# Kernel tuning notes

Hardware: AMD Instinct MI355X
Metric: run time of the kernel (lower is better)

## Reference

```python
import jax, jax.numpy as jnp
import numpy as np

N_NODES = 50000
N_REL = 1000
N_EDGES = 1600000
F_OUT = 64
N_HEAD = 2
NEG_SLOPE = 0.2


def setup_inputs() -> dict:
    key = jax.random.key(0)
    k_h, k_r, k_a0, k_a1, k_a2, k_w, k_att = jax.random.split(key, 7)
    h = jax.random.normal(k_h, (N_NODES, F_OUT), dtype=jnp.float32)
    inputr = jax.random.normal(k_r, (N_REL, F_OUT), dtype=jnp.float32)
    # A[0]=dst node, A[1]=relation id, A[2]=src node
    a0 = jax.random.randint(k_a0, (N_EDGES,), 0, N_NODES, dtype=jnp.int32)
    a1 = jax.random.randint(k_a1, (N_EDGES,), 0, N_REL, dtype=jnp.int32)
    a2 = jax.random.randint(k_a2, (N_EDGES,), 0, N_NODES, dtype=jnp.int32)
    A = jnp.stack([a0, a1, a2], axis=0)
    # params: w ~ diag per-head scale, a_src_dst ~ N(0, 1/sqrt(2*f_out))
    w = jax.random.normal(k_w, (N_HEAD - 1, 1, F_OUT), dtype=jnp.float32)
    stdv = 1.0 / np.sqrt(2 * F_OUT)
    a_src_dst = (jax.random.normal(k_att, (N_HEAD, 2, F_OUT, 1), dtype=jnp.float32) * stdv)
    return {"h": h, "inputr": inputr, "A": A, "w": w, "a_src_dst": a_src_dst}


def reference(h, inputr, A, w, a_src_dst):
    N = h.shape[0]
    dst, rel_idx, src_idx = A[0], A[1], A[2]
    outs = []
    for i in range(N_HEAD):
        if i >= 1:
            h = h * w[i - 1]  # cumulative diag rescale across heads
        src = h[src_idx]          # [E, f] gather
        rel = inputr[rel_idx]     # [E, f] gather
        score = src @ a_src_dst[i, 0] + rel @ a_src_dst[i, 1]  # [E, 1]
        edge_e = jnp.exp(-jax.nn.leaky_relu(score[:, 0], NEG_SLOPE))  # [E]
        rowsum = jax.ops.segment_sum(edge_e, dst, num_segments=N)[:, None]  # [N,1]
        msg = (src - rel) * edge_e[:, None]  # [E, f]
        h_prime = jax.ops.segment_sum(msg, dst, num_segments=N) / rowsum
        outs.append(h_prime)
    return jnp.stack(outs, axis=0)  # [n_head, N, f]
```

## Files before the change

### kernel.cpp

```cpp
#include <hip/hip_runtime.h>
#include <hip/hip_fp16.h>

#define NNODES 50000
#define NREL   1000
#define NEDGES 1600000
#define FOUT   64
#define NEG_SLOPE 0.2f

#define SPAN   16
#define NBUCK  3125
#define CAP    704
#define PTHR   1024
#define EPT    16
#define CHUNK  (PTHR * EPT)
#define DBLK   98
#define PREB   797


#define ALIGN1K(x) (((x) + 1023) & ~((size_t)1023))
static const size_t OFF_HS    = 0;
static const size_t OFF_RR    = ALIGN1K(OFF_HS    + sizeof(float2) * NNODES);
static const size_t OFF_CNT   = ALIGN1K(OFF_RR    + sizeof(float2) * NREL);
static const size_t OFF_H16   = ALIGN1K(OFF_CNT   + sizeof(int) * NBUCK);
static const size_t OFF_R16   = ALIGN1K(OFF_H16   + sizeof(unsigned short) * NNODES * FOUT);
static const size_t OFF_STAGE = ALIGN1K(OFF_R16   + sizeof(unsigned short) * NREL * FOUT);

__global__ __launch_bounds__(PTHR) void prep_kernel(
    const float* __restrict__ h, const float* __restrict__ inputr,
    const float* __restrict__ w, const float* __restrict__ a_att,
    const int* __restrict__ A, int* __restrict__ ccnt, int* __restrict__ stage,
    float2* __restrict__ hs2, float2* __restrict__ rr2,
    unsigned short* __restrict__ h16, unsigned short* __restrict__ r16)
{
    const int t = threadIdx.x;
    if (blockIdx.x < DBLK) {
        __shared__ int lcnt[NBUCK];
        __shared__ int gbase[NBUCK];
        for (int i = t; i < NBUCK; i += PTHR) lcnt[i] = 0;
        __syncthreads();

        const int base = blockIdx.x * CHUNK;
        int rec[EPT];
        short bkt[EPT];
        int off[EPT];

        #pragma unroll
        for (int k = 0; k < EPT; k++) {
            const int e = base + k * PTHR + t;
            if (e < NEDGES) {
                const int dn = __builtin_nontemporal_load(A + e);
                const int rn = __builtin_nontemporal_load(A + NEDGES + e);
                const int sn = __builtin_nontemporal_load(A + 2 * NEDGES + e);
                const int b  = dn >> 4;
                rec[k] = ((dn & 15) << 26) | (sn << 10) | rn;
                bkt[k] = (short)b;
                off[k] = atomicAdd(&lcnt[b], 1);
            } else {
                off[k] = -1;
            }
        }
        __syncthreads();

        for (int i = t; i < NBUCK; i += PTHR) {
            const int c = lcnt[i];
            if (c > 0) gbase[i] = i * CAP + atomicAdd(&ccnt[i], c);
        }
        __syncthreads();

        #pragma unroll
        for (int k = 0; k < EPT; k++) {
            if (off[k] >= 0) {
                const int b   = bkt[k];
                const int pos = gbase[b] + off[k];
                if (pos < (b + 1) * CAP)
                    stage[pos] = rec[k];
            }
        }
        return;
    }

    const int lane = t & 15;
    const int f0   = lane << 2;
    const int g    = (blockIdx.x - DBLK) * 64 + (t >> 4);
    if (g >= NNODES + NREL) return;

    const float4 a00 = *(const float4*)(a_att +   0 + f0);
    const float4 a01 = *(const float4*)(a_att +  64 + f0);
    const float4 a10 = *(const float4*)(a_att + 128 + f0);
    const float4 a11 = *(const float4*)(a_att + 192 + f0);
    const float4 wv  = *(const float4*)(w + f0);

    float p0, p1;
    float4 v;
    if (g < NNODES) {
        v = *(const float4*)(h + (size_t)g * FOUT + f0);
        p0 = v.x * a00.x + v.y * a00.y + v.z * a00.z + v.w * a00.w;
        p1 = v.x * wv.x * a10.x + v.y * wv.y * a10.y
           + v.z * wv.z * a10.z + v.w * wv.w * a10.w;
    } else {
        v = *(const float4*)(inputr + (size_t)(g - NNODES) * FOUT + f0);
        p0 = v.x * a01.x + v.y * a01.y + v.z * a01.z + v.w * a01.w;
        p1 = v.x * a11.x + v.y * a11.y + v.z * a11.z + v.w * a11.w;
    }

    {
        ushort4 pk;
        pk.x = __half_as_ushort(__float2half(v.x));
        pk.y = __half_as_ushort(__float2half(v.y));
        pk.z = __half_as_ushort(__float2half(v.z));
        pk.w = __half_as_ushort(__float2half(v.w));
        if (g < NNODES) *(ushort4*)(h16 + (size_t)g * FOUT + f0) = pk;
        else            *(ushort4*)(r16 + (size_t)(g - NNODES) * FOUT + f0) = pk;
    }

    #pragma unroll
    for (int off = 8; off >= 1; off >>= 1) {
        p0 += __shfl_xor(p0, off, 16);
        p1 += __shfl_xor(p1, off, 16);
    }
    if (lane == 0) {
        if (g < NNODES) hs2[g] = make_float2(p0, p1);
        else            rr2[g - NNODES] = make_float2(p0, p1);
    }
}

__global__ __launch_bounds__(256) void sortagg_kernel(
    const unsigned short* __restrict__ h16, const unsigned short* __restrict__ r16,
    const float* __restrict__ w,
    const int* __restrict__ stage, const int* __restrict__ ccnt,
    const float2* __restrict__ hs2, const float2* __restrict__ rr2,
    float* __restrict__ out)
{
    __shared__ int    lsort[CAP];
    __shared__ float2 ew[CAP];
    __shared__ int hist[SPAN];
    __shared__ int offs[SPAN];
    __shared__ int sstart[SPAN + 1];

    const int b = blockIdx.x;
    const int t = threadIdx.x;
    int cnt = ccnt[b];
    if (cnt > CAP) cnt = CAP;
    const int base = b * CAP;

    if (t < SPAN) hist[t] = 0;
    __syncthreads();

    for (int i = t; i < cnt; i += 256)
        atomicAdd(&hist[((unsigned)stage[base + i]) >> 26], 1);
    __syncthreads();

    if (t < SPAN) {
        const int c = hist[t];
        int v = c;
        #pragma unroll
        for (int d = 1; d < SPAN; d <<= 1) {
            const int u = __shfl_up(v, d);
            if (t >= d) v += u;
        }
        sstart[t] = v - c;
        offs[t]   = v - c;
        if (t == SPAN - 1) sstart[SPAN] = v;
    }
    __syncthreads();

    for (int i = t; i < cnt; i += 256) {
        const int r = stage[base + i];
        const int pos = atomicAdd(&offs[((unsigned)r) >> 26], 1);
        lsort[pos] = r;
        const int sn = (r >> 10) & 0xFFFF;
        const int rn = r & 1023;
        const float2 hv = hs2[sn];
        const float2 rv = rr2[rn];
        const float sc0 = hv.x + rv.x;
        const float sc1 = hv.y + rv.y;
        ew[pos] = make_float2(__expf(-fmaxf(sc0, NEG_SLOPE * sc0)),
                              __expf(-fmaxf(sc1, NEG_SLOPE * sc1)));
    }
    __syncthreads();

    const int wv  = t >> 6;
    const int oct = (t & 63) >> 3;
    const int f8  = (t & 7) << 3;
    const float4 wl0 = *(const float4*)(w + f8);
    const float4 wl1 = *(const float4*)(w + f8 + 4);

    for (int nl = wv; nl < SPAN; nl += 4) {
        const int node = b * SPAN + nl;
        const int s0 = sstart[nl];
        const int s1 = sstart[nl + 1];

        float4 a0l = make_float4(0.f, 0.f, 0.f, 0.f);
        float4 a0h = make_float4(0.f, 0.f, 0.f, 0.f);
        float4 a1l = make_float4(0.f, 0.f, 0.f, 0.f);
        float4 a1h = make_float4(0.f, 0.f, 0.f, 0.f);
        float sum0 = 0.f, sum1 = 0.f;

        for (int i = s0 + oct; i < s1; i += 8) {
            const int p     = lsort[i];
            const float2 ee = ew[i];
            const int sn = (p >> 10) & 0xFFFF;
            const int rn = p & 1023;

            const uint4 su = *(const uint4*)(h16 + ((size_t)sn << 6) + f8);
            const uint4 ru = *(const uint4*)(r16 + ((size_t)rn << 6) + f8);
            const float2 s01 = __half22float2(__builtin_bit_cast(__half2, su.x));
            const float2 s23 = __half22float2(__builtin_bit_cast(__half2, su.y));
            const float2 s45 = __half22float2(__builtin_bit_cast(__half2, su.z));
            const float2 s67 = __half22float2(__builtin_bit_cast(__half2, su.w));
            const float2 r01 = __half22float2(__builtin_bit_cast(__half2, ru.x));
            const float2 r23 = __half22float2(__builtin_bit_cast(__half2, ru.y));
            const float2 r45 = __half22float2(__builtin_bit_cast(__half2, ru.z));
            const float2 r67 = __half22float2(__builtin_bit_cast(__half2, ru.w));

            a0l.x += (s01.x - r01.x) * ee.x;
            a0l.y += (s01.y - r01.y) * ee.x;
            a0l.z += (s23.x - r23.x) * ee.x;
            a0l.w += (s23.y - r23.y) * ee.x;
            a0h.x += (s45.x - r45.x) * ee.x;
            a0h.y += (s45.y - r45.y) * ee.x;
            a0h.z += (s67.x - r67.x) * ee.x;
            a0h.w += (s67.y - r67.y) * ee.x;
            a1l.x += fmaf(s01.x, wl0.x, -r01.x) * ee.y;
            a1l.y += fmaf(s01.y, wl0.y, -r01.y) * ee.y;
            a1l.z += fmaf(s23.x, wl0.z, -r23.x) * ee.y;
            a1l.w += fmaf(s23.y, wl0.w, -r23.y) * ee.y;
            a1h.x += fmaf(s45.x, wl1.x, -r45.x) * ee.y;
            a1h.y += fmaf(s45.y, wl1.y, -r45.y) * ee.y;
            a1h.z += fmaf(s67.x, wl1.z, -r67.x) * ee.y;
            a1h.w += fmaf(s67.y, wl1.w, -r67.y) * ee.y;
            sum0 += ee.x;
            sum1 += ee.y;
        }

        #pragma unroll
        for (int off = 8; off <= 32; off <<= 1) {
            a0l.x += __shfl_xor(a0l.x, off);
            a0l.y += __shfl_xor(a0l.y, off);
            a0l.z += __shfl_xor(a0l.z, off);
            a0l.w += __shfl_xor(a0l.w, off);
            a0h.x += __shfl_xor(a0h.x, off);
            a0h.y += __shfl_xor(a0h.y, off);
            a0h.z += __shfl_xor(a0h.z, off);
            a0h.w += __shfl_xor(a0h.w, off);
            a1l.x += __shfl_xor(a1l.x, off);
            a1l.y += __shfl_xor(a1l.y, off);
            a1l.z += __shfl_xor(a1l.z, off);
            a1l.w += __shfl_xor(a1l.w, off);
            a1h.x += __shfl_xor(a1h.x, off);
            a1h.y += __shfl_xor(a1h.y, off);
            a1h.z += __shfl_xor(a1h.z, off);
            a1h.w += __shfl_xor(a1h.w, off);
            sum0   += __shfl_xor(sum0, off);
            sum1   += __shfl_xor(sum1, off);
        }

        if (oct == 0) {
            const float inv = 1.0f / sum0;
            float* o = out + (size_t)node * FOUT + f8;
            *(float4*)(o)     = make_float4(a0l.x * inv, a0l.y * inv, a0l.z * inv, a0l.w * inv);
            *(float4*)(o + 4) = make_float4(a0h.x * inv, a0h.y * inv, a0h.z * inv, a0h.w * inv);
        } else if (oct == 1) {
            const float inv = 1.0f / sum1;
            float* o = out + ((size_t)NNODES + node) * FOUT + f8;
            *(float4*)(o)     = make_float4(a1l.x * inv, a1l.y * inv, a1l.z * inv, a1l.w * inv);
            *(float4*)(o + 4) = make_float4(a1h.x * inv, a1h.y * inv, a1h.z * inv, a1h.w * inv);
        }
    }
}

extern "C" void kernel_launch(void* const* d_in, const int* in_sizes, int n_in,
                              void* d_out, int out_size, void* d_ws, size_t ws_size,
                              hipStream_t stream) {
    const float* h      = (const float*)d_in[0];
    const float* inputr = (const float*)d_in[1];
    const int*   A      = (const int*)d_in[2];
    const float* w      = (const float*)d_in[3];
    const float* a_att  = (const float*)d_in[4];

    char* ws = (char*)d_ws;
    float2*         hs2   = (float2*)(ws + OFF_HS);
    float2*         rr2   = (float2*)(ws + OFF_RR);
    int*            ccnt  = (int*)(ws + OFF_CNT);
    unsigned short* h16   = (unsigned short*)(ws + OFF_H16);
    unsigned short* r16   = (unsigned short*)(ws + OFF_R16);
    int*            stage = (int*)(ws + OFF_STAGE);
    float*          out   = (float*)d_out;

    hipMemsetAsync(ccnt, 0, sizeof(int) * NBUCK, stream);

    prep_kernel<<<dim3(DBLK + PREB), dim3(PTHR), 0, stream>>>(
        h, inputr, w, a_att, A, ccnt, stage, hs2, rr2, h16, r16);
    sortagg_kernel<<<dim3(NBUCK), dim3(256), 0, stream>>>(
        h16, r16, w, stage, ccnt, hs2, rr2, out);
}
```

Measured before the change: 88.45 us.

## Halve sortagg block size and unroll edge loop by two for more loads in flight

The aggregation kernel now runs 128-thread blocks (2 wavefronts per 16-node bucket, each handling 8 nodes) with a min-blocks-per-CU launch hint. The inner edge loop is unrolled by two so each thread issues four 16-byte gathers before consuming them, raising memory-level parallelism. The smaller block halves the threads doing the shared-memory bucket sort and makes each wave process twice as many nodes, trading thread parallelism for more blocks resident per CU. The extra in-flight loads increase register use, which the launch-bounds hint constrains.

```diff
diff --git a/kernel.cpp b/kernel.cpp
--- a/kernel.cpp
+++ b/kernel.cpp
@@ -124,7 +124,7 @@
     }
 }
 
-__global__ __launch_bounds__(256) void sortagg_kernel(
+__global__ __launch_bounds__(128, 7) void sortagg_kernel(
     const unsigned short* __restrict__ h16, const unsigned short* __restrict__ r16,
     const float* __restrict__ w,
     const int* __restrict__ stage, const int* __restrict__ ccnt,
@@ -146,7 +146,7 @@
     if (t < SPAN) hist[t] = 0;
     __syncthreads();
 
-    for (int i = t; i < cnt; i += 256)
+    for (int i = t; i < cnt; i += 128)
         atomicAdd(&hist[((unsigned)stage[base + i]) >> 26], 1);
     __syncthreads();
 
@@ -164,7 +164,7 @@
     }
     __syncthreads();
 
-    for (int i = t; i < cnt; i += 256) {
+    for (int i = t; i < cnt; i += 128) {
         const int r = stage[base + i];
         const int pos = atomicAdd(&offs[((unsigned)r) >> 26], 1);
         lsort[pos] = r;
@@ -185,7 +185,7 @@
     const float4 wl0 = *(const float4*)(w + f8);
     const float4 wl1 = *(const float4*)(w + f8 + 4);
 
-    for (int nl = wv; nl < SPAN; nl += 4) {
+    for (int nl = wv; nl < SPAN; nl += 2) {
         const int node = b * SPAN + nl;
         const int s0 = sstart[nl];
         const int s1 = sstart[nl + 1];
@@ -196,12 +196,82 @@
         float4 a1h = make_float4(0.f, 0.f, 0.f, 0.f);
         float sum0 = 0.f, sum1 = 0.f;
 
-        for (int i = s0 + oct; i < s1; i += 8) {
+        int i = s0 + oct;
+        for (; i + 8 < s1; i += 16) {
+            const int pA     = lsort[i];
+            const float2 eA  = ew[i];
+            const int pB     = lsort[i + 8];
+            const float2 eB  = ew[i + 8];
+            const int snA = (pA >> 10) & 0xFFFF, rnA = pA & 1023;
+            const int snB = (pB >> 10) & 0xFFFF, rnB = pB & 1023;
+
+            const uint4 suA = *(const uint4*)(h16 + ((size_t)snA << 6) + f8);
+            const uint4 ruA = *(const uint4*)(r16 + ((size_t)rnA << 6) + f8);
+            const uint4 suB = *(const uint4*)(h16 + ((size_t)snB << 6) + f8);
+            const uint4 ruB = *(const uint4*)(r16 + ((size_t)rnB << 6) + f8);
+
+            {
+                const float2 s01 = __half22float2(__builtin_bit_cast(__half2, suA.x));
+                const float2 s23 = __half22float2(__builtin_bit_cast(__half2, suA.y));
+                const float2 s45 = __half22float2(__builtin_bit_cast(__half2, suA.z));
+                const float2 s67 = __half22float2(__builtin_bit_cast(__half2, suA.w));
+                const float2 r01 = __half22float2(__builtin_bit_cast(__half2, ruA.x));
+                const float2 r23 = __half22float2(__builtin_bit_cast(__half2, ruA.y));
+                const float2 r45 = __half22float2(__builtin_bit_cast(__half2, ruA.z));
+                const float2 r67 = __half22float2(__builtin_bit_cast(__half2, ruA.w));
+                a0l.x += (s01.x - r01.x) * eA.x;
+                a0l.y += (s01.y - r01.y) * eA.x;
+                a0l.z += (s23.x - r23.x) * eA.x;
+                a0l.w += (s23.y - r23.y) * eA.x;
+                a0h.x += (s45.x - r45.x) * eA.x;
+                a0h.y += (s45.y - r45.y) * eA.x;
+                a0h.z += (s67.x - r67.x) * eA.x;
+                a0h.w += (s67.y - r67.y) * eA.x;
+                a1l.x += fmaf(s01.x, wl0.x, -r01.x) * eA.y;
+                a1l.y += fmaf(s01.y, wl0.y, -r01.y) * eA.y;
+                a1l.z += fmaf(s23.x, wl0.z, -r23.x) * eA.y;
+                a1l.w += fmaf(s23.y, wl0.w, -r23.y) * eA.y;
+                a1h.x += fmaf(s45.x, wl1.x, -r45.x) * eA.y;
+                a1h.y += fmaf(s45.y, wl1.y, -r45.y) * eA.y;
+                a1h.z += fmaf(s67.x, wl1.z, -r67.x) * eA.y;
+                a1h.w += fmaf(s67.y, wl1.w, -r67.y) * eA.y;
+                sum0 += eA.x;
+                sum1 += eA.y;
+            }
+            {
+                const float2 s01 = __half22float2(__builtin_bit_cast(__half2, suB.x));
+                const float2 s23 = __half22float2(__builtin_bit_cast(__half2, suB.y));
+                const float2 s45 = __half22float2(__builtin_bit_cast(__half2, suB.z));
+                const float2 s67 = __half22float2(__builtin_bit_cast(__half2, suB.w));
+                const float2 r01 = __half22float2(__builtin_bit_cast(__half2, ruB.x));
+                const float2 r23 = __half22float2(__builtin_bit_cast(__half2, ruB.y));
+                const float2 r45 = __half22float2(__builtin_bit_cast(__half2, ruB.z));
+                const float2 r67 = __half22float2(__builtin_bit_cast(__half2, ruB.w));
+                a0l.x += (s01.x - r01.x) * eB.x;
+                a0l.y += (s01.y - r01.y) * eB.x;
+                a0l.z += (s23.x - r23.x) * eB.x;
+                a0l.w += (s23.y - r23.y) * eB.x;
+                a0h.x += (s45.x - r45.x) * eB.x;
+                a0h.y += (s45.y - r45.y) * eB.x;
+                a0h.z += (s67.x - r67.x) * eB.x;
+                a0h.w += (s67.y - r67.y) * eB.x;
+                a1l.x += fmaf(s01.x, wl0.x, -r01.x) * eB.y;
+                a1l.y += fmaf(s01.y, wl0.y, -r01.y) * eB.y;
+                a1l.z += fmaf(s23.x, wl0.z, -r23.x) * eB.y;
+                a1l.w += fmaf(s23.y, wl0.w, -r23.y) * eB.y;
+                a1h.x += fmaf(s45.x, wl1.x, -r45.x) * eB.y;
+                a1h.y += fmaf(s45.y, wl1.y, -r45.y) * eB.y;
+                a1h.z += fmaf(s67.x, wl1.z, -r67.x) * eB.y;
+                a1h.w += fmaf(s67.y, wl1.w, -r67.y) * eB.y;
+                sum0 += eB.x;
+                sum1 += eB.y;
+            }
+        }
+        if (i < s1) {
             const int p     = lsort[i];
             const float2 ee = ew[i];
             const int sn = (p >> 10) & 0xFFFF;
             const int rn = p & 1023;
-
             const uint4 su = *(const uint4*)(h16 + ((size_t)sn << 6) + f8);
             const uint4 ru = *(const uint4*)(r16 + ((size_t)rn << 6) + f8);
             const float2 s01 = __half22float2(__builtin_bit_cast(__half2, su.x));
@@ -212,7 +282,6 @@
             const float2 r23 = __half22float2(__builtin_bit_cast(__half2, ru.y));
             const float2 r45 = __half22float2(__builtin_bit_cast(__half2, ru.z));
             const float2 r67 = __half22float2(__builtin_bit_cast(__half2, ru.w));
-
             a0l.x += (s01.x - r01.x) * ee.x;
             a0l.y += (s01.y - r01.y) * ee.x;
             a0l.z += (s23.x - r23.x) * ee.x;
@@ -291,6 +360,6 @@
 
     prep_kernel<<<dim3(DBLK + PREB), dim3(PTHR), 0, stream>>>(
         h, inputr, w, a_att, A, ccnt, stage, hs2, rr2, h16, r16);
-    sortagg_kernel<<<dim3(NBUCK), dim3(256), 0, stream>>>(
+    sortagg_kernel<<<dim3(NBUCK), dim3(128), 0, stream>>>(
         h16, r16, w, stage, ccnt, hs2, rr2, out);
 }
```

After: 92.29 us. 1.04x slower.
